# Optimization experiments

Measured on AMD Instinct MI355X. Metric: run time of the kernel, lower is better.

The kernel has to match this reference:

```python
import jax, jax.numpy as jnp
import numpy as np

BINS = 2048
DST_NBINS = 8
STEP = 1e-5


def _get_norm(delta_begin, delta_end, density):
    # integral of x^2 * density over [delta_begin, delta_end]
    return density * (delta_end ** 3 - delta_begin ** 3) / 3.0


def _quant_error(hist, bin_width, nsb, neb):
    # L2 quantization error of mapping src bins [nsb, neb] onto DST_NBINS bins
    dst_w = bin_width * (neb - nsb + 1).astype(jnp.float32) / DST_NBINS
    safe_w = jnp.where(dst_w == 0.0, 1.0, dst_w)
    src = jnp.arange(BINS, dtype=jnp.float32)
    begin = (src - nsb) * bin_width          # src bin left edge rel. to new range
    end = begin + bin_width
    db = jnp.clip(jnp.floor(begin / safe_w), 0, DST_NBINS - 1)
    de = jnp.clip(jnp.floor(end / safe_w), 0, DST_NBINS - 1)
    density = hist / bin_width
    db_c = (db + 0.5) * safe_w
    norm = _get_norm(begin - db_c, safe_w / 2, density)
    norm = norm + (de - db - 1.0) * _get_norm(-safe_w / 2, safe_w / 2, density)
    de_c = de * safe_w + safe_w / 2
    norm = norm + _get_norm(-safe_w / 2, end - de_c, density)
    return jnp.where(dst_w == 0.0, jnp.float32(0.0), norm.sum())


def _search(hist, min_val, max_val):
    # entropy-style greedy shrink of [start_bin, end_bin]; sequential, data-dependent
    bin_width = (max_val - min_val) / BINS
    total = hist.sum()
    cSum = jnp.cumsum(hist)

    def cond(s):
        alpha, beta, sb, eb, nm, done = s
        return (alpha < beta) & jnp.logical_not(done)

    def body(s):
        alpha, beta, sb, eb, nm, done = s
        na = alpha + STEP
        nb = beta - STEP
        # l: first bin (>= sb) with cSum >= na*total; r: last bin with cSum <= nb*total
        l = jnp.clip(jnp.searchsorted(cSum, na * total, side='left'), sb, eb)
        r = jnp.clip(jnp.searchsorted(cSum, nb * total, side='right') - 1, sb, eb)
        take_left = (l - sb) > (eb - r)
        nsb = jnp.where(take_left, l, sb)
        neb = jnp.where(take_left, eb, r)
        alpha2 = jnp.where(take_left, na, alpha)
        beta2 = jnp.where(take_left, beta, nb)
        changed = (nsb != sb) | (neb != eb)
        norm = _quant_error(hist, bin_width, nsb, neb)
        broke = changed & (norm > nm)
        accept = changed & jnp.logical_not(broke)
        return (alpha2, beta2,
                jnp.where(accept, nsb, sb),
                jnp.where(accept, neb, eb),
                jnp.where(accept, norm, nm),
                done | broke)

    init = (jnp.float32(0.0), jnp.float32(1.0),
            jnp.int32(0), jnp.int32(BINS - 1),
            jnp.float32(jnp.inf), jnp.bool_(False))
    _, _, sb, eb, _, _ = jax.lax.while_loop(cond, body, init)
    return sb, eb


def _forward(x):
    min_val = jnp.min(x)
    max_val = jnp.max(x)
    bin_width = (max_val - min_val) / BINS
    safe_bw = jnp.where(bin_width == 0.0, 1.0, bin_width)
    # torch.histc equivalent over [min_val, max_val]
    idx = jnp.clip(jnp.floor((x.ravel() - min_val) / safe_bw).astype(jnp.int32), 0, BINS - 1)
    hist = jnp.zeros(BINS, jnp.float32).at[idx].add(1.0)
    sb, eb = _search(jax.lax.stop_gradient(hist),
                     jax.lax.stop_gradient(min_val),
                     jax.lax.stop_gradient(max_val))
    new_min = min_val + bin_width * sb
    new_max = min_val + bin_width * (eb + 1)
    return jnp.stack([new_min, new_max])


def setup_inputs() -> dict:
    key = jax.random.key(0)
    x = jax.random.normal(key, (32, 1024, 1024), dtype=jnp.float32)
    return {"x": x}


def reference(x):
    return _forward(x)
```

## Files before the change

kernel.cpp:

```cpp
#include <hip/hip_runtime.h>
#include <float.h>
#include <math.h>

#define BINS 2048
#define DSTN 8
#define STEPF 1e-5f
#define NMM 1024
#define NHIST 512
#define MAXST 2048
#define NSEG 64
#define MINF 0x7fffffff
#define NT 1024

struct Ws {
  unsigned int mm_done, ev_done;
  int nseg, mbot;
  int n_states;
  int pad0[3];
  float min_val, max_val, bin_width, safe_bw;
  float pmin[NMM];
  float pmax[NMM];
  unsigned int hist[BINS];
  float histf[BINS];
  float Atab[2052];
  int   mterm[2052];
  int4  segB4[NSEG];
  float norms[MAXST];
  int2  states[MAXST];
};

__global__ void __launch_bounds__(256) k_minmax(const float* __restrict__ x, long long n,
                                                Ws* __restrict__ ws) {
  __shared__ float smin[4], smax[4];
  __shared__ float redn[256], redx[256];
  __shared__ __align__(16) int4 sB4[NSEG], sA4[NSEG];
  __shared__ int segklo[NSEG];
  __shared__ int s_nsg, s_mbot, s_nsa;
  __shared__ int amLast;
  int t = threadIdx.x;
  const float S = STEPF;

  if (blockIdx.x == NMM) {
    if (t == 0) {
      int sg = 0; float B = 1.0f; int m0 = 0; int mbot = MINF;
      while (sg < NSEG && B > 0.0f) {
        float Bn = B - S;
        if (Bn <= 0.0f) {
          sB4[sg] = make_int4(__float_as_int(B), __float_as_int(B - Bn), m0, 0);
          ++sg; mbot = m0 + 1; break;
        }
        float d = B - Bn;
        unsigned bb = __float_as_uint(B);
        unsigned bid = bb & 0x7f800000u;
        if ((bb & 0x007fffffu) == 0u) bid -= 0x00800000u;
        float binlo = __uint_as_float(bid);
        float brel = B - binlo;
        int nn = (int)floor((double)brel / (double)d);
        if (nn < 0) nn = 0;
        if (nn >= 2) {
          float B1 = B - d;
          float B2 = B1 - S;
          if (B1 - B2 != d) nn = 1;
        }
        sB4[sg] = make_int4(__float_as_int(B), __float_as_int(d), m0, nn);
        ++sg;
        float Blast = B - (float)nn * d;
        B = Blast - S;
        m0 += nn + 1;
        if (B <= 0.0f) { mbot = m0; break; }
      }
      s_nsg = sg; s_mbot = mbot;
      int sa = 0;
      sA4[sa++] = make_int4(__float_as_int(0.0f), __float_as_int(S), 0, 0);
      float A0 = S; int k0 = 1;
      while (sa < NSEG && k0 <= 2051) {
        float An = A0 + S;
        float d = An - A0;
        unsigned ab = __float_as_uint(A0);
        unsigned abid = ab & 0x7f800000u;
        float binhi = __uint_as_float(abid + 0x00800000u);
        float brel = binhi - A0;
        int nn = (int)floorf(brel / d);
        if (nn < 0) nn = 0;
        while (nn >= 1 && !(A0 + (float)nn * d < binhi)) --nn;
        while (A0 + (float)(nn + 1) * d < binhi) ++nn;
        if (nn >= 2) {
          float A1 = A0 + d;
          float A2 = A1 + S;
          if (A2 - A1 != d) nn = 1;
        }
        if (k0 + nn > 2051) nn = 2051 - k0;
        sA4[sa++] = make_int4(__float_as_int(A0), __float_as_int(d), k0, nn);
        float Alast = A0 + (float)nn * d;
        A0 = Alast + S;
        k0 += nn + 1;
      }
      s_nsa = sa;
    }
    __syncthreads();
    int nsg = s_nsg, mbot = s_mbot, nsa = s_nsa;

    for (int sg = 0; sg < nsa; ++sg) {
      int4 sv = sA4[sg];
      float A0v = __int_as_float(sv.x), dv = __int_as_float(sv.y);
      for (int i = t; i <= sv.w; i += 256) ws->Atab[sv.z + i] = A0v + (float)i * dv;
    }
    __syncthreads();
    {
      int okA = 1;
      for (int k = t; k < 2051; k += 256) okA &= (ws->Atab[k] + S == ws->Atab[k + 1]) ? 1 : 0;
      if (__syncthreads_and(okA) == 0) {
        if (t == 0) {
          float a = 0.0f; ws->Atab[0] = 0.0f;
          for (int k = 1; k < 2052; ++k) { a = a + S; ws->Atab[k] = a; }
        }
        __syncthreads();
      }
    }
    if (t < nsg) {
      int4 sv = sB4[t];
      float Bs = __int_as_float(sv.x), dd = __int_as_float(sv.y);
      float Bend = Bs - (float)sv.w * dd;
      int lo = 0, hi = 2052;
      while (lo < hi) { int mid = (lo + hi) >> 1; if (ws->Atab[mid] < Bend) lo = mid + 1; else hi = mid; }
      segklo[t] = lo;
      ws->segB4[t] = sv;
    }
    if (t == 0) { ws->nseg = nsg; ws->mbot = mbot; }
    __syncthreads();
    for (int sg = 0; sg < nsg; ++sg) {
      int lo = segklo[sg], hi = (sg ? segklo[sg - 1] : 2052);
      if (lo >= hi) continue;
      int4 sv = sB4[sg];
      float Bs = __int_as_float(sv.x), dd = __int_as_float(sv.y);
      int ms = sv.z, nn = sv.w;
      float rd = (dd > 0.0f) ? 1.0f / dd : 0.0f;
      for (int k = lo + t; k < hi; k += 256) {
        float a = ws->Atab[k];
        int i2 = (int)((Bs - a) * rd);
        if (i2 < 0) i2 = 0; if (i2 > nn) i2 = nn;
        while (i2 > 0 && Bs - (float)(i2 - 1) * dd <= a) --i2;
        while (i2 <= nn && Bs - (float)i2 * dd > a) ++i2;
        ws->mterm[k] = ms + i2;
      }
    }
    {
      int dhi = segklo[nsg - 1];
      for (int k = t; k < dhi; k += 256) ws->mterm[k] = mbot;
    }
    return;
  }

  long long n4 = n >> 2;
  float vmin = FLT_MAX, vmax = -FLT_MAX;
  const float4* __restrict__ x4 = (const float4*)x;
  long long stride = (long long)NMM * blockDim.x;
  for (long long i = (long long)blockIdx.x * blockDim.x + t; i < n4; i += stride) {
    float4 v = x4[i];
    vmin = fminf(vmin, fminf(fminf(v.x, v.y), fminf(v.z, v.w)));
    vmax = fmaxf(vmax, fmaxf(fmaxf(v.x, v.y), fmaxf(v.z, v.w)));
  }
  for (long long i = (n4 << 2) + (long long)blockIdx.x * blockDim.x + t; i < n; i += stride) {
    float v = x[i];
    vmin = fminf(vmin, v); vmax = fmaxf(vmax, v);
  }
  for (int off = 32; off > 0; off >>= 1) {
    vmin = fminf(vmin, __shfl_down(vmin, off));
    vmax = fmaxf(vmax, __shfl_down(vmax, off));
  }
  int wid = t >> 6;
  if ((t & 63) == 0) { smin[wid] = vmin; smax[wid] = vmax; }
  __syncthreads();
  if (t == 0) {
    float a = smin[0], b = smax[0];
    for (int w = 1; w < 4; ++w) { a = fminf(a, smin[w]); b = fmaxf(b, smax[w]); }
    ws->pmin[blockIdx.x] = a; ws->pmax[blockIdx.x] = b;
    __threadfence();
    amLast = (atomicAdd(&ws->mm_done, 1u) == (unsigned)(NMM - 1)) ? 1 : 0;
  }
  __syncthreads();
  if (amLast) {
    __threadfence();
    float fmn = FLT_MAX, fmx = -FLT_MAX;
    for (int i = t; i < NMM; i += 256) {
      fmn = fminf(fmn, ws->pmin[i]);
      fmx = fmaxf(fmx, ws->pmax[i]);
    }
    redn[t] = fmn; redx[t] = fmx;
    __syncthreads();
    for (int off = 128; off > 0; off >>= 1) {
      if (t < off) { redn[t] = fminf(redn[t], redn[t + off]); redx[t] = fmaxf(redx[t], redx[t + off]); }
      __syncthreads();
    }
    if (t == 0) {
      float mn = redn[0], mx = redx[0];
      ws->min_val = mn; ws->max_val = mx;
      float bw = (mx - mn) / (float)BINS;
      ws->bin_width = bw;
      ws->safe_bw = (bw == 0.0f) ? 1.0f : bw;
    }
    for (int i = t; i < BINS; i += 256) ws->hist[i] = 0u;
  }
}

__global__ void __launch_bounds__(256) k_hist(const float* __restrict__ x, long long n,
                                              Ws* __restrict__ ws) {
  __shared__ __align__(16) unsigned int lh[BINS * 4];
  for (int i = threadIdx.x; i < BINS * 4; i += 256) lh[i] = 0u;
  __syncthreads();
  float minv = ws->min_val;
  float sbw = ws->safe_bw;
  int sub = threadIdx.x & 3;
  long long n4 = n >> 2;
  const float4* __restrict__ x4 = (const float4*)x;
  long long stride = (long long)gridDim.x * blockDim.x;
  for (long long i = (long long)blockIdx.x * blockDim.x + threadIdx.x; i < n4; i += stride) {
    float4 v = x4[i];
    int a = (int)floorf((v.x - minv) / sbw);
    int b = (int)floorf((v.y - minv) / sbw);
    int c = (int)floorf((v.z - minv) / sbw);
    int d = (int)floorf((v.w - minv) / sbw);
    a = min(BINS - 1, max(0, a));
    b = min(BINS - 1, max(0, b));
    c = min(BINS - 1, max(0, c));
    d = min(BINS - 1, max(0, d));
    atomicAdd(&lh[(a << 2) | sub], 1u);
    atomicAdd(&lh[(b << 2) | sub], 1u);
    atomicAdd(&lh[(c << 2) | sub], 1u);
    atomicAdd(&lh[(d << 2) | sub], 1u);
  }
  for (long long i = (n4 << 2) + (long long)blockIdx.x * blockDim.x + threadIdx.x; i < n; i += stride) {
    int a = (int)floorf((x[i] - minv) / sbw);
    a = min(BINS - 1, max(0, a));
    atomicAdd(&lh[(a << 2) | sub], 1u);
  }
  __syncthreads();
  for (int i = threadIdx.x; i < BINS; i += 256) {
    uint4 v = *((const uint4*)lh + i);
    unsigned int c = v.x + v.y + v.z + v.w;
    if (c) atomicAdd(&ws->hist[i], c);
  }
}

__global__ void __launch_bounds__(NT) k_search(Ws* __restrict__ ws) {
  __shared__ __align__(16) float csum[BINS];
  __shared__ __align__(16) int2  ltmt[2052];
  __shared__ __align__(16) int   mcross[BINS];
  __shared__ __align__(16) int   chain[2052];
  __shared__ __align__(16) int2  ev[2049];
  __shared__ __align__(16) int4  sB4[NSEG];
  __shared__ int   segblo[NSEG];
  __shared__ float fwav[16];
  __shared__ int   ired[16], ired2[16];
  __shared__ int   pub_nc;
  __shared__ int   pub_mode, pub_j0, pub_sb, pub_mt, pub_nst0, pub_nfire, pub_clamp, pub_ntot;

  int t = threadIdx.x;
  int lane = t & 63, wid = t >> 6;

  if (t < NSEG) sB4[t] = ws->segB4[t];
  int nsg = ws->nseg;
  int mbot = ws->mbot;

  float h0 = (float)ws->hist[2 * t];
  float h1 = (float)ws->hist[2 * t + 1];
  ws->histf[2 * t] = h0; ws->histf[2 * t + 1] = h1;
  float s = h0 + h1;
  float isc = s;
  #pragma unroll
  for (int off = 1; off < 64; off <<= 1) {
    float u = __shfl_up(isc, off);
    if (lane >= off) isc += u;
  }
  if (lane == 63) fwav[wid] = isc;
  __syncthreads();
  if (t < 16) {
    float v = fwav[t];
    #pragma unroll
    for (int off = 1; off < 16; off <<= 1) {
      float u = __shfl_up(v, off, 16);
      if ((t & 15) >= off) v += u;
    }
    fwav[t] = v;
  }
  __syncthreads();
  {
    float base = wid ? fwav[wid - 1] : 0.0f;
    float excl = base + (isc - s);
    csum[2 * t] = excl + h0;
    csum[2 * t + 1] = excl + s;
  }
  __syncthreads();

  const float T = csum[BINS - 1];
  const float rcpT = 1.0f / T;

  {
    int lov[3], hiv[3];
    float av1[3];
    #pragma unroll
    for (int i = 0; i < 3; ++i) {
      int k = t + NT * i;
      bool has = (k <= 2050);
      lov[i] = 0; hiv[i] = has ? BINS : 0;
      av1[i] = has ? ws->Atab[k + 1] * T : 0.0f;
    }
    #pragma unroll
    for (int lev = 0; lev < 12; ++lev) {
      #pragma unroll
      for (int i = 0; i < 3; ++i) {
        bool act = lov[i] < hiv[i];
        int mid = act ? ((lov[i] + hiv[i]) >> 1) : 0;
        float cv = csum[mid];
        bool g = act && (cv < av1[i]);
        lov[i] = g ? (mid + 1) : lov[i];
        hiv[i] = (act && !g) ? mid : hiv[i];
      }
    }
    #pragma unroll
    for (int i = 0; i < 3; ++i) {
      int k = t + NT * i;
      if (k < 2052) ltmt[k] = make_int2((k <= 2050) ? lov[i] : BINS, ws->mterm[k]);
    }
  }
  if (t < nsg) {
    int4 sv = sB4[t];
    float Bs = __int_as_float(sv.x), dd = __int_as_float(sv.y);
    float Bend = Bs - (float)sv.w * dd;
    float vt = Bend * T;
    int lo = 0, hi = BINS;
    while (lo < hi) { int mid = (lo + hi) >> 1; if (!(csum[mid] > vt)) lo = mid + 1; else hi = mid; }
    segblo[t] = lo;
  }
  __syncthreads();

  for (int sg = 0; sg < nsg; ++sg) {
    int lo = segblo[sg], hi = (sg ? segblo[sg - 1] : BINS);
    if (lo >= hi) continue;
    int4 sv = sB4[sg];
    float Bs = __int_as_float(sv.x), dd = __int_as_float(sv.y);
    int ms = sv.z, nn = sv.w;
    float rd = (dd > 0.0f) ? 1.0f / dd : 0.0f;
    for (int b = lo + t; b < hi; b += NT) {
      float c = csum[b];
      int i2 = (int)((Bs - c * rcpT) * rd);
      if (i2 < 0) i2 = 0; if (i2 > nn) i2 = nn;
      while (i2 > 0 && (Bs - (float)(i2 - 1) * dd) * T < c) --i2;
      while (i2 <= nn && !((Bs - (float)i2 * dd) * T < c)) ++i2;
      mcross[b] = ms + i2 - 1;
    }
  }
  {
    int dhi = segblo[nsg - 1];
    for (int b = t; b < dhi; b += NT) {
      float c = csum[b];
      mcross[b] = (c > 0.0f) ? ((mbot == MINF) ? MINF : (mbot - 1)) : MINF;
    }
  }
  __syncthreads();

  {
    int b0 = 2 * t;
    int m0v = mcross[b0], m1v = mcross[b0 + 1];
    int mnext = (t < NT - 1) ? mcross[b0 + 2] : 0;
    bool e0b = (m0v != m1v);
    bool e1b = (b0 + 1 == BINS - 1) || (m1v != mnext);
    int cnt = (e0b ? 1 : 0) + (e1b ? 1 : 0);
    int inc = cnt;
    #pragma unroll
    for (int off = 1; off < 64; off <<= 1) {
      int u = __shfl_up(inc, off);
      if (lane >= off) inc += u;
    }
    if (lane == 63) ired[wid] = inc;
    __syncthreads();
    if (t < 16) {
      int v = ired[t];
      #pragma unroll
      for (int off = 1; off < 16; off <<= 1) {
        int u = __shfl_up(v, off, 16);
        if ((t & 15) >= off) v += u;
      }
      ired[t] = v;
    }
    __syncthreads();
    int base = wid ? ired[wid - 1] : 0;
    int incl_t = base + inc;
    int total = ired[15];
    int running = total - incl_t;
    if (e1b) { ++running; chain[running - 1] = b0 + 1; }
    if (e0b) { ++running; chain[running - 1] = b0; }
    if (t == 0) pub_nc = total;
  }
  __syncthreads();

  int NC = pub_nc;
  for (int j = 1 + t; j <= NC; j += NT) {
    ev[j] = make_int2(mcross[chain[j - 1]], (j < NC) ? chain[j] : -1);
  }
  if (t == 0 && NC < 2048) ev[NC + 1] = make_int2(MINF, -1);
  __syncthreads();

  if (t == 0) {
    int k = 0, sb = 0, eb = BINS - 1, m = 0, j = 1, nst = 0;
    int2 lm0 = ltmt[0], lm1 = ltmt[1], lm2 = ltmt[2];
    int2 e0 = ev[1], e1 = ev[2], e2 = ev[3];
    int mode = 0;
    int guard = 0;
    pub_j0 = 0; pub_sb = 0; pub_mt = 0;
    while (++guard < 6000) {
      int lpos = lm0.x, mt = lm0.y;
      int mc = e0.x, ne = e0.y;
      int l = min(lpos, eb);
      int pl = l - sb;
      if (pl <= 0) { mode = 1; pub_j0 = j; pub_sb = sb; pub_mt = mt; break; }
      if (m >= mt) break;
      bool coin = (m == mc);
      int nec = max(ne, sb);
      int pr = eb - nec;
      bool fl = !coin || (pl > pr);
      if (fl) {
        sb = l; ++k;
        if (nst < MAXST) ws->states[nst] = make_int2(sb, eb);
        ++nst;
        if (sb >= eb) break;
        lm0 = lm1; lm1 = lm2; lm2 = ltmt[min(k + 2, 2051)];
      } else {
        eb = nec; m = mc + 1; ++j;
        if (nst < MAXST) ws->states[nst] = make_int2(sb, eb);
        ++nst;
        if (sb >= eb) break;
        e0 = e1; e1 = e2; e2 = ev[min(j + 2, 2048)];
      }
    }
    pub_mode = mode;
    pub_nst0 = (nst < MAXST) ? nst : MAXST;
  }
  __syncthreads();

  int mode = pub_mode;
  int nst0 = pub_nst0;
  if (mode == 1) {
    int j0 = pub_j0, sbF = pub_sb, mtF = pub_mt;
    int locA = NC + 1, locB = NC + 1;
    for (int j = j0 + t; j <= NC; j += NT) {
      int2 e = ev[j];
      if (e.x >= mtF && j < locA) locA = j;
      if (e.y <= sbF && j < locB) locB = j;
    }
    #pragma unroll
    for (int off = 32; off > 0; off >>= 1) {
      locA = min(locA, __shfl_down(locA, off));
      locB = min(locB, __shfl_down(locB, off));
    }
    if (lane == 0) { ired[wid] = locA; ired2[wid] = locB; }
    __syncthreads();
    if (t == 0) {
      int jA = NC + 1, jB = NC + 1;
      for (int w = 0; w < 16; ++w) { jA = min(jA, ired[w]); jB = min(jB, ired2[w]); }
      int nfire, clampLast;
      if (jB < jA) { nfire = jB - j0 + 1; clampLast = 1; }
      else         { nfire = jA - j0;     clampLast = 0; }
      if (nfire < 0) nfire = 0;
      int ntot = nst0 + nfire;
      if (ntot > MAXST) ntot = MAXST;
      pub_nfire = nfire; pub_clamp = clampLast; pub_ntot = ntot;
    }
    __syncthreads();
    int nfire = pub_nfire, clampLast = pub_clamp;
    for (int i = t; i < nfire; i += NT) {
      int idx = nst0 + i;
      if (idx < MAXST) {
        int y = ev[j0 + i].y;
        ws->states[idx] = make_int2(sbF, (clampLast && i == nfire - 1) ? sbF : y);
      }
    }
    if (t == 0) ws->n_states = pub_ntot;
  } else {
    if (t == 0) ws->n_states = nst0;
  }
}

__global__ void __launch_bounds__(256) k_eval(Ws* __restrict__ ws) {
  int i = blockIdx.x;
  if (i >= ws->n_states) return;
  int2 st = ws->states[i];
  float bw = ws->bin_width;
  float cntf = (float)(st.y - st.x + 1);
  float w = bw * cntf / (float)DSTN;
  int t = threadIdx.x;
  if (w == 0.0f) {
    if (t == 0) ws->norms[i] = 0.0f;
    return;
  }
  float hw = 0.5f * w;
  float hw3 = hw * hw * hw;
  float nsb = (float)st.x;
  float sum = 0.0f;
  #pragma unroll
  for (int k = 0; k < 8; ++k) {
    int j = t + 256 * k;
    float h = ws->histf[j];
    float begin = ((float)j - nsb) * bw;
    float end = begin + bw;
    float db = fminf(fmaxf(floorf(begin / w), 0.0f), (float)(DSTN - 1));
    float de = fminf(fmaxf(floorf(end / w), 0.0f), (float)(DSTN - 1));
    float density = h / bw;
    float dbc = (db + 0.5f) * w;
    float a1 = begin - dbc;
    float n1 = density * (hw3 - a1 * a1 * a1) / 3.0f;
    float nmid = density * (hw3 + hw3) / 3.0f;
    float dec = de * w + hw;
    float a3 = end - dec;
    float n3 = density * (a3 * a3 * a3 + hw3) / 3.0f;
    sum += n1 + (de - db - 1.0f) * nmid + n3;
  }
  __shared__ float red[256];
  red[t] = sum;
  __syncthreads();
  for (int off = 128; off > 0; off >>= 1) {
    if (t < off) red[t] += red[t + off];
    __syncthreads();
  }
  if (t == 0) ws->norms[i] = red[0];
}

__global__ void __launch_bounds__(256) k_final(Ws* __restrict__ ws, float* __restrict__ out) {
  __shared__ int sbrk[256];
  int N = ws->n_states;
  int t = threadIdx.x;
  int loc = MINF;
  for (int i = t + 1; i < N; i += 256) {
    if (ws->norms[i] > ws->norms[i - 1]) loc = min(loc, i);
  }
  sbrk[t] = loc;
  __syncthreads();
  for (int off = 128; off > 0; off >>= 1) {
    if (t < off) sbrk[t] = min(sbrk[t], sbrk[t + off]);
    __syncthreads();
  }
  if (t == 0) {
    int sb, eb;
    if (N == 0) { sb = 0; eb = BINS - 1; }
    else {
      int ib = sbrk[0];
      int fi = (ib != MINF) ? (ib - 1) : (N - 1);
      int2 st = ws->states[fi];
      sb = st.x; eb = st.y;
    }
    float minv = ws->min_val, bw = ws->bin_width;
    out[0] = minv + bw * (float)sb;
    out[1] = minv + bw * (float)(eb + 1);
  }
}

extern "C" void kernel_launch(void* const* d_in, const int* in_sizes, int n_in,
                              void* d_out, int out_size, void* d_ws, size_t ws_size,
                              hipStream_t stream) {
  const float* x = (const float*)d_in[0];
  long long n = (long long)in_sizes[0];
  Ws* ws = (Ws*)d_ws;
  float* out = (float*)d_out;

  hipMemsetAsync(d_ws, 0, 8, stream);
  k_minmax<<<NMM + 1, 256, 0, stream>>>(x, n, ws);
  k_hist<<<NHIST, 256, 0, stream>>>(x, n, ws);
  k_search<<<1, NT, 0, stream>>>(ws);
  k_eval<<<MAXST, 256, 0, stream>>>(ws);
  k_final<<<1, 256, 0, stream>>>(ws, out);
}
```

Measured before the change: 165.2 us.

## Split table build into its own kernel and unroll min/max and histogram loads

The float-step table construction moves out of the extra k_minmax block into a separate single-block kernel launched first, so k_minmax no longer has one slow serial block holding up its tail. The min/max loop is unrolled four ways and the histogram loop two ways, so more independent float4 loads are in flight per thread. A reciprocal-multiply histogram variant is added but not launched. The launched k_hist_exact keeps the exact division. The cost is one more kernel launch, and the table kernel now runs serially ahead of the min/max pass.

```diff
diff --git a/kernel.cpp b/kernel.cpp
--- a/kernel.cpp
+++ b/kernel.cpp
@@ -29,139 +29,157 @@
   int2  states[MAXST];
 };
 
+__global__ void __launch_bounds__(256) k_tables(Ws* __restrict__ ws) {
+  __shared__ __align__(16) int4 sB4[NSEG], sA4[NSEG];
+  __shared__ int segklo[NSEG];
+  __shared__ int s_nsg, s_mbot, s_nsa;
+  int t = threadIdx.x;
+  const float S = STEPF;
+
+  if (t == 0) {
+    int sg = 0; float B = 1.0f; int m0 = 0; int mbot = MINF;
+    while (sg < NSEG && B > 0.0f) {
+      float Bn = B - S;
+      if (Bn <= 0.0f) {
+        sB4[sg] = make_int4(__float_as_int(B), __float_as_int(B - Bn), m0, 0);
+        ++sg; mbot = m0 + 1; break;
+      }
+      float d = B - Bn;
+      unsigned bb = __float_as_uint(B);
+      unsigned bid = bb & 0x7f800000u;
+      if ((bb & 0x007fffffu) == 0u) bid -= 0x00800000u;
+      float binlo = __uint_as_float(bid);
+      float brel = B - binlo;
+      int nn = (int)floor((double)brel / (double)d);
+      if (nn < 0) nn = 0;
+      if (nn >= 2) {
+        float B1 = B - d;
+        float B2 = B1 - S;
+        if (B1 - B2 != d) nn = 1;
+      }
+      sB4[sg] = make_int4(__float_as_int(B), __float_as_int(d), m0, nn);
+      ++sg;
+      float Blast = B - (float)nn * d;
+      B = Blast - S;
+      m0 += nn + 1;
+      if (B <= 0.0f) { mbot = m0; break; }
+    }
+    s_nsg = sg; s_mbot = mbot;
+    int sa = 0;
+    sA4[sa++] = make_int4(__float_as_int(0.0f), __float_as_int(S), 0, 0);
+    float A0 = S; int k0 = 1;
+    while (sa < NSEG && k0 <= 2051) {
+      float An = A0 + S;
+      float d = An - A0;
+      unsigned ab = __float_as_uint(A0);
+      unsigned abid = ab & 0x7f800000u;
+      float binhi = __uint_as_float(abid + 0x00800000u);
+      float brel = binhi - A0;
+      int nn = (int)floorf(brel / d);
+      if (nn < 0) nn = 0;
+      while (nn >= 1 && !(A0 + (float)nn * d < binhi)) --nn;
+      while (A0 + (float)(nn + 1) * d < binhi) ++nn;
+      if (nn >= 2) {
+        float A1 = A0 + d;
+        float A2 = A1 + S;
+        if (A2 - A1 != d) nn = 1;
+      }
+      if (k0 + nn > 2051) nn = 2051 - k0;
+      sA4[sa++] = make_int4(__float_as_int(A0), __float_as_int(d), k0, nn);
+      float Alast = A0 + (float)nn * d;
+      A0 = Alast + S;
+      k0 += nn + 1;
+    }
+    s_nsa = sa;
+  }
+  __syncthreads();
+  int nsg = s_nsg, mbot = s_mbot, nsa = s_nsa;
+
+  for (int sg = 0; sg < nsa; ++sg) {
+    int4 sv = sA4[sg];
+    float A0v = __int_as_float(sv.x), dv = __int_as_float(sv.y);
+    for (int i = t; i <= sv.w; i += 256) ws->Atab[sv.z + i] = A0v + (float)i * dv;
+  }
+  __syncthreads();
+  {
+    int okA = 1;
+    for (int k = t; k < 2051; k += 256) okA &= (ws->Atab[k] + S == ws->Atab[k + 1]) ? 1 : 0;
+    if (__syncthreads_and(okA) == 0) {
+      if (t == 0) {
+        float a = 0.0f; ws->Atab[0] = 0.0f;
+        for (int k = 1; k < 2052; ++k) { a = a + S; ws->Atab[k] = a; }
+      }
+      __syncthreads();
+    }
+  }
+  if (t < nsg) {
+    int4 sv = sB4[t];
+    float Bs = __int_as_float(sv.x), dd = __int_as_float(sv.y);
+    float Bend = Bs - (float)sv.w * dd;
+    int lo = 0, hi = 2052;
+    while (lo < hi) { int mid = (lo + hi) >> 1; if (ws->Atab[mid] < Bend) lo = mid + 1; else hi = mid; }
+    segklo[t] = lo;
+    ws->segB4[t] = sv;
+  }
+  if (t == 0) { ws->nseg = nsg; ws->mbot = mbot; }
+  __syncthreads();
+  for (int sg = 0; sg < nsg; ++sg) {
+    int lo = segklo[sg], hi = (sg ? segklo[sg - 1] : 2052);
+    if (lo >= hi) continue;
+    int4 sv = sB4[sg];
+    float Bs = __int_as_float(sv.x), dd = __int_as_float(sv.y);
+    int ms = sv.z, nn = sv.w;
+    float rd = (dd > 0.0f) ? 1.0f / dd : 0.0f;
+    for (int k = lo + t; k < hi; k += 256) {
+      float a = ws->Atab[k];
+      int i2 = (int)((Bs - a) * rd);
+      if (i2 < 0) i2 = 0; if (i2 > nn) i2 = nn;
+      while (i2 > 0 && Bs - (float)(i2 - 1) * dd <= a) --i2;
+      while (i2 <= nn && Bs - (float)i2 * dd > a) ++i2;
+      ws->mterm[k] = ms + i2;
+    }
+  }
+  {
+    int dhi = segklo[nsg - 1];
+    for (int k = t; k < dhi; k += 256) ws->mterm[k] = mbot;
+  }
+}
+
 __global__ void __launch_bounds__(256) k_minmax(const float* __restrict__ x, long long n,
                                                 Ws* __restrict__ ws) {
   __shared__ float smin[4], smax[4];
   __shared__ float redn[256], redx[256];
-  __shared__ __align__(16) int4 sB4[NSEG], sA4[NSEG];
-  __shared__ int segklo[NSEG];
-  __shared__ int s_nsg, s_mbot, s_nsa;
   __shared__ int amLast;
   int t = threadIdx.x;
-  const float S = STEPF;
-
-  if (blockIdx.x == NMM) {
-    if (t == 0) {
-      int sg = 0; float B = 1.0f; int m0 = 0; int mbot = MINF;
-      while (sg < NSEG && B > 0.0f) {
-        float Bn = B - S;
-        if (Bn <= 0.0f) {
-          sB4[sg] = make_int4(__float_as_int(B), __float_as_int(B - Bn), m0, 0);
-          ++sg; mbot = m0 + 1; break;
-        }
-        float d = B - Bn;
-        unsigned bb = __float_as_uint(B);
-        unsigned bid = bb & 0x7f800000u;
-        if ((bb & 0x007fffffu) == 0u) bid -= 0x00800000u;
-        float binlo = __uint_as_float(bid);
-        float brel = B - binlo;
-        int nn = (int)floor((double)brel / (double)d);
-        if (nn < 0) nn = 0;
-        if (nn >= 2) {
-          float B1 = B - d;
-          float B2 = B1 - S;
-          if (B1 - B2 != d) nn = 1;
-        }
-        sB4[sg] = make_int4(__float_as_int(B), __float_as_int(d), m0, nn);
-        ++sg;
-        float Blast = B - (float)nn * d;
-        B = Blast - S;
-        m0 += nn + 1;
-        if (B <= 0.0f) { mbot = m0; break; }
-      }
-      s_nsg = sg; s_mbot = mbot;
-      int sa = 0;
-      sA4[sa++] = make_int4(__float_as_int(0.0f), __float_as_int(S), 0, 0);
-      float A0 = S; int k0 = 1;
-      while (sa < NSEG && k0 <= 2051) {
-        float An = A0 + S;
-        float d = An - A0;
-        unsigned ab = __float_as_uint(A0);
-        unsigned abid = ab & 0x7f800000u;
-        float binhi = __uint_as_float(abid + 0x00800000u);
-        float brel = binhi - A0;
-        int nn = (int)floorf(brel / d);
-        if (nn < 0) nn = 0;
-        while (nn >= 1 && !(A0 + (float)nn * d < binhi)) --nn;
-        while (A0 + (float)(nn + 1) * d < binhi) ++nn;
-        if (nn >= 2) {
-          float A1 = A0 + d;
-          float A2 = A1 + S;
-          if (A2 - A1 != d) nn = 1;
-        }
-        if (k0 + nn > 2051) nn = 2051 - k0;
-        sA4[sa++] = make_int4(__float_as_int(A0), __float_as_int(d), k0, nn);
-        float Alast = A0 + (float)nn * d;
-        A0 = Alast + S;
-        k0 += nn + 1;
-      }
-      s_nsa = sa;
-    }
-    __syncthreads();
-    int nsg = s_nsg, mbot = s_mbot, nsa = s_nsa;
-
-    for (int sg = 0; sg < nsa; ++sg) {
-      int4 sv = sA4[sg];
-      float A0v = __int_as_float(sv.x), dv = __int_as_float(sv.y);
-      for (int i = t; i <= sv.w; i += 256) ws->Atab[sv.z + i] = A0v + (float)i * dv;
-    }
-    __syncthreads();
-    {
-      int okA = 1;
-      for (int k = t; k < 2051; k += 256) okA &= (ws->Atab[k] + S == ws->Atab[k + 1]) ? 1 : 0;
-      if (__syncthreads_and(okA) == 0) {
-        if (t == 0) {
-          float a = 0.0f; ws->Atab[0] = 0.0f;
-          for (int k = 1; k < 2052; ++k) { a = a + S; ws->Atab[k] = a; }
-        }
-        __syncthreads();
-      }
-    }
-    if (t < nsg) {
-      int4 sv = sB4[t];
-      float Bs = __int_as_float(sv.x), dd = __int_as_float(sv.y);
-      float Bend = Bs - (float)sv.w * dd;
-      int lo = 0, hi = 2052;
-      while (lo < hi) { int mid = (lo + hi) >> 1; if (ws->Atab[mid] < Bend) lo = mid + 1; else hi = mid; }
-      segklo[t] = lo;
-      ws->segB4[t] = sv;
-    }
-    if (t == 0) { ws->nseg = nsg; ws->mbot = mbot; }
-    __syncthreads();
-    for (int sg = 0; sg < nsg; ++sg) {
-      int lo = segklo[sg], hi = (sg ? segklo[sg - 1] : 2052);
-      if (lo >= hi) continue;
-      int4 sv = sB4[sg];
-      float Bs = __int_as_float(sv.x), dd = __int_as_float(sv.y);
-      int ms = sv.z, nn = sv.w;
-      float rd = (dd > 0.0f) ? 1.0f / dd : 0.0f;
-      for (int k = lo + t; k < hi; k += 256) {
-        float a = ws->Atab[k];
-        int i2 = (int)((Bs - a) * rd);
-        if (i2 < 0) i2 = 0; if (i2 > nn) i2 = nn;
-        while (i2 > 0 && Bs - (float)(i2 - 1) * dd <= a) --i2;
-        while (i2 <= nn && Bs - (float)i2 * dd > a) ++i2;
-        ws->mterm[k] = ms + i2;
-      }
-    }
-    {
-      int dhi = segklo[nsg - 1];
-      for (int k = t; k < dhi; k += 256) ws->mterm[k] = mbot;
-    }
-    return;
-  }
 
   long long n4 = n >> 2;
   float vmin = FLT_MAX, vmax = -FLT_MAX;
   const float4* __restrict__ x4 = (const float4*)x;
-  long long stride = (long long)NMM * blockDim.x;
-  for (long long i = (long long)blockIdx.x * blockDim.x + t; i < n4; i += stride) {
+  const long long stride = (long long)NMM * 256;
+  long long i = (long long)blockIdx.x * 256 + t;
+  for (; i + 3 * stride < n4; i += 4 * stride) {
+    float4 v0 = x4[i];
+    float4 v1 = x4[i + stride];
+    float4 v2 = x4[i + 2 * stride];
+    float4 v3 = x4[i + 3 * stride];
+    float mn0 = fminf(fminf(v0.x, v0.y), fminf(v0.z, v0.w));
+    float mx0 = fmaxf(fmaxf(v0.x, v0.y), fmaxf(v0.z, v0.w));
+    float mn1 = fminf(fminf(v1.x, v1.y), fminf(v1.z, v1.w));
+    float mx1 = fmaxf(fmaxf(v1.x, v1.y), fmaxf(v1.z, v1.w));
+    float mn2 = fminf(fminf(v2.x, v2.y), fminf(v2.z, v2.w));
+    float mx2 = fmaxf(fmaxf(v2.x, v2.y), fmaxf(v2.z, v2.w));
+    float mn3 = fminf(fminf(v3.x, v3.y), fminf(v3.z, v3.w));
+    float mx3 = fmaxf(fmaxf(v3.x, v3.y), fmaxf(v3.z, v3.w));
+    vmin = fminf(vmin, fminf(fminf(mn0, mn1), fminf(mn2, mn3)));
+    vmax = fmaxf(vmax, fmaxf(fmaxf(mx0, mx1), fmaxf(mx2, mx3)));
+  }
+  for (; i < n4; i += stride) {
     float4 v = x4[i];
     vmin = fminf(vmin, fminf(fminf(v.x, v.y), fminf(v.z, v.w)));
     vmax = fmaxf(vmax, fmaxf(fmaxf(v.x, v.y), fmaxf(v.z, v.w)));
   }
-  for (long long i = (n4 << 2) + (long long)blockIdx.x * blockDim.x + t; i < n; i += stride) {
-    float v = x[i];
+  for (long long q = (n4 << 2) + (long long)blockIdx.x * 256 + t; q < n; q += stride) {
+    float v = x[q];
     vmin = fminf(vmin, v); vmax = fmaxf(vmax, v);
   }
   for (int off = 32; off > 0; off >>= 1) {
@@ -182,9 +200,9 @@
   if (amLast) {
     __threadfence();
     float fmn = FLT_MAX, fmx = -FLT_MAX;
-    for (int i = t; i < NMM; i += 256) {
-      fmn = fminf(fmn, ws->pmin[i]);
-      fmx = fmaxf(fmx, ws->pmax[i]);
+    for (int q = t; q < NMM; q += 256) {
+      fmn = fminf(fmn, ws->pmin[q]);
+      fmx = fmaxf(fmx, ws->pmax[q]);
     }
     redn[t] = fmn; redx[t] = fmx;
     __syncthreads();
@@ -199,12 +217,70 @@
       ws->bin_width = bw;
       ws->safe_bw = (bw == 0.0f) ? 1.0f : bw;
     }
-    for (int i = t; i < BINS; i += 256) ws->hist[i] = 0u;
+    for (int q = t; q < BINS; q += 256) ws->hist[q] = 0u;
   }
 }
 
 __global__ void __launch_bounds__(256) k_hist(const float* __restrict__ x, long long n,
                                               Ws* __restrict__ ws) {
+  __shared__ __align__(16) unsigned int lh[BINS * 4];
+  for (int i = threadIdx.x; i < BINS * 4; i += 256) lh[i] = 0u;
+  __syncthreads();
+  float minv = ws->min_val;
+  float sbw = ws->safe_bw;
+  float rbw = 1.0f / sbw;
+  int sub = threadIdx.x & 3;
+  long long n4 = n >> 2;
+  const float4* __restrict__ x4 = (const float4*)x;
+  const long long stride = (long long)NHIST * 256;
+  long long i = (long long)blockIdx.x * 256 + threadIdx.x;
+  for (; i + stride < n4; i += 2 * stride) {
+    float4 v0 = x4[i];
+    float4 v1 = x4[i + stride];
+    int a0 = min(BINS - 1, max(0, (int)floorf((v0.x - minv) * rbw)));
+    int b0 = min(BINS - 1, max(0, (int)floorf((v0.y - minv) * rbw)));
+    int c0 = min(BINS - 1, max(0, (int)floorf((v0.z - minv) * rbw)));
+    int d0 = min(BINS - 1, max(0, (int)floorf((v0.w - minv) * rbw)));
+    int a1 = min(BINS - 1, max(0, (int)floorf((v1.x - minv) * rbw)));
+    int b1 = min(BINS - 1, max(0, (int)floorf((v1.y - minv) * rbw)));
+    int c1 = min(BINS - 1, max(0, (int)floorf((v1.z - minv) * rbw)));
+    int d1 = min(BINS - 1, max(0, (int)floorf((v1.w - minv) * rbw)));
+    atomicAdd(&lh[(a0 << 2) | sub], 1u);
+    atomicAdd(&lh[(b0 << 2) | sub], 1u);
+    atomicAdd(&lh[(c0 << 2) | sub], 1u);
+    atomicAdd(&lh[(d0 << 2) | sub], 1u);
+    atomicAdd(&lh[(a1 << 2) | sub], 1u);
+    atomicAdd(&lh[(b1 << 2) | sub], 1u);
+    atomicAdd(&lh[(c1 << 2) | sub], 1u);
+    atomicAdd(&lh[(d1 << 2) | sub], 1u);
+  }
+  for (; i < n4; i += stride) {
+    float4 v = x4[i];
+    int a = min(BINS - 1, max(0, (int)floorf((v.x - minv) * rbw)));
+    int b = min(BINS - 1, max(0, (int)floorf((v.y - minv) * rbw)));
+    int c = min(BINS - 1, max(0, (int)floorf((v.z - minv) * rbw)));
+    int d = min(BINS - 1, max(0, (int)floorf((v.w - minv) * rbw)));
+    atomicAdd(&lh[(a << 2) | sub], 1u);
+    atomicAdd(&lh[(b << 2) | sub], 1u);
+    atomicAdd(&lh[(c << 2) | sub], 1u);
+    atomicAdd(&lh[(d << 2) | sub], 1u);
+  }
+  for (long long q = (n4 << 2) + (long long)blockIdx.x * 256 + threadIdx.x; q < n; q += stride) {
+    int a = (int)floorf((x[q] - minv) / sbw);
+    a = min(BINS - 1, max(0, a));
+    atomicAdd(&lh[(a << 2) | sub], 1u);
+  }
+  __syncthreads();
+  for (int q = threadIdx.x; q < BINS; q += 256) {
+    uint4 v = *((const uint4*)lh + q);
+    unsigned int c = v.x + v.y + v.z + v.w;
+    if (c) atomicAdd(&ws->hist[q], c);
+  }
+}
+
+
+__global__ void __launch_bounds__(256) k_hist_exact(const float* __restrict__ x, long long n,
+                                                    Ws* __restrict__ ws) {
   __shared__ __align__(16) unsigned int lh[BINS * 4];
   for (int i = threadIdx.x; i < BINS * 4; i += 256) lh[i] = 0u;
   __syncthreads();
@@ -213,32 +289,49 @@
   int sub = threadIdx.x & 3;
   long long n4 = n >> 2;
   const float4* __restrict__ x4 = (const float4*)x;
-  long long stride = (long long)gridDim.x * blockDim.x;
-  for (long long i = (long long)blockIdx.x * blockDim.x + threadIdx.x; i < n4; i += stride) {
+  const long long stride = (long long)NHIST * 256;
+  long long i = (long long)blockIdx.x * 256 + threadIdx.x;
+  for (; i + stride < n4; i += 2 * stride) {
+    float4 v0 = x4[i];
+    float4 v1 = x4[i + stride];
+    int a0 = min(BINS - 1, max(0, (int)floorf((v0.x - minv) / sbw)));
+    int b0 = min(BINS - 1, max(0, (int)floorf((v0.y - minv) / sbw)));
+    int c0 = min(BINS - 1, max(0, (int)floorf((v0.z - minv) / sbw)));
+    int d0 = min(BINS - 1, max(0, (int)floorf((v0.w - minv) / sbw)));
+    int a1 = min(BINS - 1, max(0, (int)floorf((v1.x - minv) / sbw)));
+    int b1 = min(BINS - 1, max(0, (int)floorf((v1.y - minv) / sbw)));
+    int c1 = min(BINS - 1, max(0, (int)floorf((v1.z - minv) / sbw)));
+    int d1 = min(BINS - 1, max(0, (int)floorf((v1.w - minv) / sbw)));
+    atomicAdd(&lh[(a0 << 2) | sub], 1u);
+    atomicAdd(&lh[(b0 << 2) | sub], 1u);
+    atomicAdd(&lh[(c0 << 2) | sub], 1u);
+    atomicAdd(&lh[(d0 << 2) | sub], 1u);
+    atomicAdd(&lh[(a1 << 2) | sub], 1u);
+    atomicAdd(&lh[(b1 << 2) | sub], 1u);
+    atomicAdd(&lh[(c1 << 2) | sub], 1u);
+    atomicAdd(&lh[(d1 << 2) | sub], 1u);
+  }
+  for (; i < n4; i += stride) {
     float4 v = x4[i];
-    int a = (int)floorf((v.x - minv) / sbw);
-    int b = (int)floorf((v.y - minv) / sbw);
-    int c = (int)floorf((v.z - minv) / sbw);
-    int d = (int)floorf((v.w - minv) / sbw);
-    a = min(BINS - 1, max(0, a));
-    b = min(BINS - 1, max(0, b));
-    c = min(BINS - 1, max(0, c));
-    d = min(BINS - 1, max(0, d));
+    int a = min(BINS - 1, max(0, (int)floorf((v.x - minv) / sbw)));
+    int b = min(BINS - 1, max(0, (int)floorf((v.y - minv) / sbw)));
+    int c = min(BINS - 1, max(0, (int)floorf((v.z - minv) / sbw)));
+    int d = min(BINS - 1, max(0, (int)floorf((v.w - minv) / sbw)));
     atomicAdd(&lh[(a << 2) | sub], 1u);
     atomicAdd(&lh[(b << 2) | sub], 1u);
     atomicAdd(&lh[(c << 2) | sub], 1u);
     atomicAdd(&lh[(d << 2) | sub], 1u);
   }
-  for (long long i = (n4 << 2) + (long long)blockIdx.x * blockDim.x + threadIdx.x; i < n; i += stride) {
-    int a = (int)floorf((x[i] - minv) / sbw);
+  for (long long q = (n4 << 2) + (long long)blockIdx.x * 256 + threadIdx.x; q < n; q += stride) {
+    int a = (int)floorf((x[q] - minv) / sbw);
     a = min(BINS - 1, max(0, a));
     atomicAdd(&lh[(a << 2) | sub], 1u);
   }
   __syncthreads();
-  for (int i = threadIdx.x; i < BINS; i += 256) {
-    uint4 v = *((const uint4*)lh + i);
+  for (int q = threadIdx.x; q < BINS; q += 256) {
+    uint4 v = *((const uint4*)lh + q);
     unsigned int c = v.x + v.y + v.z + v.w;
-    if (c) atomicAdd(&ws->hist[i], c);
+    if (c) atomicAdd(&ws->hist[q], c);
   }
 }
 
@@ -563,8 +656,9 @@
   float* out = (float*)d_out;
 
   hipMemsetAsync(d_ws, 0, 8, stream);
-  k_minmax<<<NMM + 1, 256, 0, stream>>>(x, n, ws);
-  k_hist<<<NHIST, 256, 0, stream>>>(x, n, ws);
+  k_tables<<<1, 256, 0, stream>>>(ws);
+  k_minmax<<<NMM, 256, 0, stream>>>(x, n, ws);
+  k_hist_exact<<<NHIST, 256, 0, stream>>>(x, n, ws);
   k_search<<<1, NT, 0, stream>>>(ws);
   k_eval<<<MAXST, 256, 0, stream>>>(ws);
   k_final<<<1, 256, 0, stream>>>(ws, out);
```

Result: slower. 186.3 us (+12.8%).

## Split table build into own kernel; contiguous chunked, unrolled minmax and histogram loads

Applied to the files above, without the earlier changes.

Moves the serial table-construction work out of the minmax grid into its own single-block kernel, so the minmax blocks no longer wait on a straggler block. Both the minmax and histogram kernels now give each block one contiguous chunk and unroll the loads (8 and 4 float4 per iteration) to keep more memory requests in flight. NMM doubles to 2048 and launch bounds hint at 2 blocks per CU. The price is an extra kernel launch that runs serially before minmax, plus longer per-thread register live ranges.

```diff
diff --git a/kernel.cpp b/kernel.cpp
--- a/kernel.cpp
+++ b/kernel.cpp
@@ -5,7 +5,7 @@
 #define BINS 2048
 #define DSTN 8
 #define STEPF 1e-5f
-#define NMM 1024
+#define NMM 2048
 #define NHIST 512
 #define MAXST 2048
 #define NSEG 64
@@ -29,141 +29,180 @@
   int2  states[MAXST];
 };
 
-__global__ void __launch_bounds__(256) k_minmax(const float* __restrict__ x, long long n,
-                                                Ws* __restrict__ ws) {
-  __shared__ float smin[4], smax[4];
-  __shared__ float redn[256], redx[256];
+__global__ void __launch_bounds__(256) k_tables(Ws* __restrict__ ws) {
   __shared__ __align__(16) int4 sB4[NSEG], sA4[NSEG];
   __shared__ int segklo[NSEG];
   __shared__ int s_nsg, s_mbot, s_nsa;
+  int t = threadIdx.x;
+  const float S = STEPF;
+
+  if (t == 0) {
+    int sg = 0; float B = 1.0f; int m0 = 0; int mbot = MINF;
+    while (sg < NSEG && B > 0.0f) {
+      float Bn = B - S;
+      if (Bn <= 0.0f) {
+        sB4[sg] = make_int4(__float_as_int(B), __float_as_int(B - Bn), m0, 0);
+        ++sg; mbot = m0 + 1; break;
+      }
+      float d = B - Bn;
+      unsigned bb = __float_as_uint(B);
+      unsigned bid = bb & 0x7f800000u;
+      if ((bb & 0x007fffffu) == 0u) bid -= 0x00800000u;
+      float binlo = __uint_as_float(bid);
+      float brel = B - binlo;
+      int nn = (int)floor((double)brel / (double)d);
+      if (nn < 0) nn = 0;
+      if (nn >= 2) {
+        float B1 = B - d;
+        float B2 = B1 - S;
+        if (B1 - B2 != d) nn = 1;
+      }
+      sB4[sg] = make_int4(__float_as_int(B), __float_as_int(d), m0, nn);
+      ++sg;
+      float Blast = B - (float)nn * d;
+      B = Blast - S;
+      m0 += nn + 1;
+      if (B <= 0.0f) { mbot = m0; break; }
+    }
+    s_nsg = sg; s_mbot = mbot;
+    int sa = 0;
+    sA4[sa++] = make_int4(__float_as_int(0.0f), __float_as_int(S), 0, 0);
+    float A0 = S; int k0 = 1;
+    while (sa < NSEG && k0 <= 2051) {
+      float An = A0 + S;
+      float d = An - A0;
+      unsigned ab = __float_as_uint(A0);
+      unsigned abid = ab & 0x7f800000u;
+      float binhi = __uint_as_float(abid + 0x00800000u);
+      float brel = binhi - A0;
+      int nn = (int)floorf(brel / d);
+      if (nn < 0) nn = 0;
+      while (nn >= 1 && !(A0 + (float)nn * d < binhi)) --nn;
+      while (A0 + (float)(nn + 1) * d < binhi) ++nn;
+      if (nn >= 2) {
+        float A1 = A0 + d;
+        float A2 = A1 + S;
+        if (A2 - A1 != d) nn = 1;
+      }
+      if (k0 + nn > 2051) nn = 2051 - k0;
+      sA4[sa++] = make_int4(__float_as_int(A0), __float_as_int(d), k0, nn);
+      float Alast = A0 + (float)nn * d;
+      A0 = Alast + S;
+      k0 += nn + 1;
+    }
+    s_nsa = sa;
+  }
+  __syncthreads();
+  int nsg = s_nsg, mbot = s_mbot, nsa = s_nsa;
+
+  for (int sg = 0; sg < nsa; ++sg) {
+    int4 sv = sA4[sg];
+    float A0v = __int_as_float(sv.x), dv = __int_as_float(sv.y);
+    for (int i = t; i <= sv.w; i += 256) ws->Atab[sv.z + i] = A0v + (float)i * dv;
+  }
+  __syncthreads();
+  {
+    int okA = 1;
+    for (int k = t; k < 2051; k += 256) okA &= (ws->Atab[k] + S == ws->Atab[k + 1]) ? 1 : 0;
+    if (__syncthreads_and(okA) == 0) {
+      if (t == 0) {
+        float a = 0.0f; ws->Atab[0] = 0.0f;
+        for (int k = 1; k < 2052; ++k) { a = a + S; ws->Atab[k] = a; }
+      }
+      __syncthreads();
+    }
+  }
+  if (t < nsg) {
+    int4 sv = sB4[t];
+    float Bs = __int_as_float(sv.x), dd = __int_as_float(sv.y);
+    float Bend = Bs - (float)sv.w * dd;
+    int lo = 0, hi = 2052;
+    while (lo < hi) { int mid = (lo + hi) >> 1; if (ws->Atab[mid] < Bend) lo = mid + 1; else hi = mid; }
+    segklo[t] = lo;
+    ws->segB4[t] = sv;
+  }
+  if (t == 0) { ws->nseg = nsg; ws->mbot = mbot; }
+  __syncthreads();
+  for (int sg = 0; sg < nsg; ++sg) {
+    int lo = segklo[sg], hi = (sg ? segklo[sg - 1] : 2052);
+    if (lo >= hi) continue;
+    int4 sv = sB4[sg];
+    float Bs = __int_as_float(sv.x), dd = __int_as_float(sv.y);
+    int ms = sv.z, nn = sv.w;
+    float rd = (dd > 0.0f) ? 1.0f / dd : 0.0f;
+    for (int k = lo + t; k < hi; k += 256) {
+      float a = ws->Atab[k];
+      int i2 = (int)((Bs - a) * rd);
+      if (i2 < 0) i2 = 0; if (i2 > nn) i2 = nn;
+      while (i2 > 0 && Bs - (float)(i2 - 1) * dd <= a) --i2;
+      while (i2 <= nn && Bs - (float)i2 * dd > a) ++i2;
+      ws->mterm[k] = ms + i2;
+    }
+  }
+  {
+    int dhi = segklo[nsg - 1];
+    for (int k = t; k < dhi; k += 256) ws->mterm[k] = mbot;
+  }
+}
+
+__global__ void __launch_bounds__(256, 2) k_minmax(const float* __restrict__ x, long long n,
+                                                   Ws* __restrict__ ws) {
+  __shared__ float smin[4], smax[4];
+  __shared__ float redn[256], redx[256];
   __shared__ int amLast;
   int t = threadIdx.x;
-  const float S = STEPF;
-
-  if (blockIdx.x == NMM) {
-    if (t == 0) {
-      int sg = 0; float B = 1.0f; int m0 = 0; int mbot = MINF;
-      while (sg < NSEG && B > 0.0f) {
-        float Bn = B - S;
-        if (Bn <= 0.0f) {
-          sB4[sg] = make_int4(__float_as_int(B), __float_as_int(B - Bn), m0, 0);
-          ++sg; mbot = m0 + 1; break;
-        }
-        float d = B - Bn;
-        unsigned bb = __float_as_uint(B);
-        unsigned bid = bb & 0x7f800000u;
-        if ((bb & 0x007fffffu) == 0u) bid -= 0x00800000u;
-        float binlo = __uint_as_float(bid);
-        float brel = B - binlo;
-        int nn = (int)floor((double)brel / (double)d);
-        if (nn < 0) nn = 0;
-        if (nn >= 2) {
-          float B1 = B - d;
-          float B2 = B1 - S;
-          if (B1 - B2 != d) nn = 1;
-        }
-        sB4[sg] = make_int4(__float_as_int(B), __float_as_int(d), m0, nn);
-        ++sg;
-        float Blast = B - (float)nn * d;
-        B = Blast - S;
-        m0 += nn + 1;
-        if (B <= 0.0f) { mbot = m0; break; }
-      }
-      s_nsg = sg; s_mbot = mbot;
-      int sa = 0;
-      sA4[sa++] = make_int4(__float_as_int(0.0f), __float_as_int(S), 0, 0);
-      float A0 = S; int k0 = 1;
-      while (sa < NSEG && k0 <= 2051) {
-        float An = A0 + S;
-        float d = An - A0;
-        unsigned ab = __float_as_uint(A0);
-        unsigned abid = ab & 0x7f800000u;
-        float binhi = __uint_as_float(abid + 0x00800000u);
-        float brel = binhi - A0;
-        int nn = (int)floorf(brel / d);
-        if (nn < 0) nn = 0;
-        while (nn >= 1 && !(A0 + (float)nn * d < binhi)) --nn;
-        while (A0 + (float)(nn + 1) * d < binhi) ++nn;
-        if (nn >= 2) {
-          float A1 = A0 + d;
-          float A2 = A1 + S;
-          if (A2 - A1 != d) nn = 1;
-        }
-        if (k0 + nn > 2051) nn = 2051 - k0;
-        sA4[sa++] = make_int4(__float_as_int(A0), __float_as_int(d), k0, nn);
-        float Alast = A0 + (float)nn * d;
-        A0 = Alast + S;
-        k0 += nn + 1;
-      }
-      s_nsa = sa;
-    }
-    __syncthreads();
-    int nsg = s_nsg, mbot = s_mbot, nsa = s_nsa;
-
-    for (int sg = 0; sg < nsa; ++sg) {
-      int4 sv = sA4[sg];
-      float A0v = __int_as_float(sv.x), dv = __int_as_float(sv.y);
-      for (int i = t; i <= sv.w; i += 256) ws->Atab[sv.z + i] = A0v + (float)i * dv;
-    }
-    __syncthreads();
-    {
-      int okA = 1;
-      for (int k = t; k < 2051; k += 256) okA &= (ws->Atab[k] + S == ws->Atab[k + 1]) ? 1 : 0;
-      if (__syncthreads_and(okA) == 0) {
-        if (t == 0) {
-          float a = 0.0f; ws->Atab[0] = 0.0f;
-          for (int k = 1; k < 2052; ++k) { a = a + S; ws->Atab[k] = a; }
-        }
-        __syncthreads();
-      }
-    }
-    if (t < nsg) {
-      int4 sv = sB4[t];
-      float Bs = __int_as_float(sv.x), dd = __int_as_float(sv.y);
-      float Bend = Bs - (float)sv.w * dd;
-      int lo = 0, hi = 2052;
-      while (lo < hi) { int mid = (lo + hi) >> 1; if (ws->Atab[mid] < Bend) lo = mid + 1; else hi = mid; }
-      segklo[t] = lo;
-      ws->segB4[t] = sv;
-    }
-    if (t == 0) { ws->nseg = nsg; ws->mbot = mbot; }
-    __syncthreads();
-    for (int sg = 0; sg < nsg; ++sg) {
-      int lo = segklo[sg], hi = (sg ? segklo[sg - 1] : 2052);
-      if (lo >= hi) continue;
-      int4 sv = sB4[sg];
-      float Bs = __int_as_float(sv.x), dd = __int_as_float(sv.y);
-      int ms = sv.z, nn = sv.w;
-      float rd = (dd > 0.0f) ? 1.0f / dd : 0.0f;
-      for (int k = lo + t; k < hi; k += 256) {
-        float a = ws->Atab[k];
-        int i2 = (int)((Bs - a) * rd);
-        if (i2 < 0) i2 = 0; if (i2 > nn) i2 = nn;
-        while (i2 > 0 && Bs - (float)(i2 - 1) * dd <= a) --i2;
-        while (i2 <= nn && Bs - (float)i2 * dd > a) ++i2;
-        ws->mterm[k] = ms + i2;
-      }
-    }
-    {
-      int dhi = segklo[nsg - 1];
-      for (int k = t; k < dhi; k += 256) ws->mterm[k] = mbot;
-    }
-    return;
-  }
 
   long long n4 = n >> 2;
+  const float4* __restrict__ x4 = (const float4*)x;
+  long long chunk = (n4 + NMM - 1) / NMM;
+  long long end = (long long)(blockIdx.x + 1) * chunk;
+  if (end > n4) end = n4;
+  long long i = (long long)blockIdx.x * chunk + t;
   float vmin = FLT_MAX, vmax = -FLT_MAX;
-  const float4* __restrict__ x4 = (const float4*)x;
-  long long stride = (long long)NMM * blockDim.x;
-  for (long long i = (long long)blockIdx.x * blockDim.x + t; i < n4; i += stride) {
+
+  for (; i + 7 * 256 < end; i += 8 * 256) {
+    float4 v0 = x4[i];
+    float4 v1 = x4[i + 256];
+    float4 v2 = x4[i + 512];
+    float4 v3 = x4[i + 768];
+    float4 v4 = x4[i + 1024];
+    float4 v5 = x4[i + 1280];
+    float4 v6 = x4[i + 1536];
+    float4 v7 = x4[i + 1792];
+    float mn0 = fminf(fminf(v0.x, v0.y), fminf(v0.z, v0.w));
+    float mn1 = fminf(fminf(v1.x, v1.y), fminf(v1.z, v1.w));
+    float mn2 = fminf(fminf(v2.x, v2.y), fminf(v2.z, v2.w));
+    float mn3 = fminf(fminf(v3.x, v3.y), fminf(v3.z, v3.w));
+    float mn4 = fminf(fminf(v4.x, v4.y), fminf(v4.z, v4.w));
+    float mn5 = fminf(fminf(v5.x, v5.y), fminf(v5.z, v5.w));
+    float mn6 = fminf(fminf(v6.x, v6.y), fminf(v6.z, v6.w));
+    float mn7 = fminf(fminf(v7.x, v7.y), fminf(v7.z, v7.w));
+    float mx0 = fmaxf(fmaxf(v0.x, v0.y), fmaxf(v0.z, v0.w));
+    float mx1 = fmaxf(fmaxf(v1.x, v1.y), fmaxf(v1.z, v1.w));
+    float mx2 = fmaxf(fmaxf(v2.x, v2.y), fmaxf(v2.z, v2.w));
+    float mx3 = fmaxf(fmaxf(v3.x, v3.y), fmaxf(v3.z, v3.w));
+    float mx4 = fmaxf(fmaxf(v4.x, v4.y), fmaxf(v4.z, v4.w));
+    float mx5 = fmaxf(fmaxf(v5.x, v5.y), fmaxf(v5.z, v5.w));
+    float mx6 = fmaxf(fmaxf(v6.x, v6.y), fmaxf(v6.z, v6.w));
+    float mx7 = fmaxf(fmaxf(v7.x, v7.y), fmaxf(v7.z, v7.w));
+    vmin = fminf(vmin, fminf(fminf(fminf(mn0, mn1), fminf(mn2, mn3)),
+                             fminf(fminf(mn4, mn5), fminf(mn6, mn7))));
+    vmax = fmaxf(vmax, fmaxf(fmaxf(fmaxf(mx0, mx1), fmaxf(mx2, mx3)),
+                             fmaxf(fmaxf(mx4, mx5), fmaxf(mx6, mx7))));
+  }
+  for (; i < end; i += 256) {
     float4 v = x4[i];
     vmin = fminf(vmin, fminf(fminf(v.x, v.y), fminf(v.z, v.w)));
     vmax = fmaxf(vmax, fmaxf(fmaxf(v.x, v.y), fmaxf(v.z, v.w)));
   }
-  for (long long i = (n4 << 2) + (long long)blockIdx.x * blockDim.x + t; i < n; i += stride) {
-    float v = x[i];
-    vmin = fminf(vmin, v); vmax = fmaxf(vmax, v);
-  }
+  if (blockIdx.x == 0) {
+    int rem = (int)(n - (n4 << 2));
+    if (t < rem) {
+      float v = x[(n4 << 2) + t];
+      vmin = fminf(vmin, v); vmax = fmaxf(vmax, v);
+    }
+  }
+
   for (int off = 32; off > 0; off >>= 1) {
     vmin = fminf(vmin, __shfl_down(vmin, off));
     vmax = fmaxf(vmax, __shfl_down(vmax, off));
@@ -182,9 +221,9 @@
   if (amLast) {
     __threadfence();
     float fmn = FLT_MAX, fmx = -FLT_MAX;
-    for (int i = t; i < NMM; i += 256) {
-      fmn = fminf(fmn, ws->pmin[i]);
-      fmx = fmaxf(fmx, ws->pmax[i]);
+    for (int q = t; q < NMM; q += 256) {
+      fmn = fminf(fmn, ws->pmin[q]);
+      fmx = fmaxf(fmx, ws->pmax[q]);
     }
     redn[t] = fmn; redx[t] = fmx;
     __syncthreads();
@@ -199,46 +238,88 @@
       ws->bin_width = bw;
       ws->safe_bw = (bw == 0.0f) ? 1.0f : bw;
     }
-    for (int i = t; i < BINS; i += 256) ws->hist[i] = 0u;
+    for (int q = t; q < BINS; q += 256) ws->hist[q] = 0u;
   }
 }
 
-__global__ void __launch_bounds__(256) k_hist(const float* __restrict__ x, long long n,
-                                              Ws* __restrict__ ws) {
+__global__ void __launch_bounds__(256, 2) k_hist(const float* __restrict__ x, long long n,
+                                                 Ws* __restrict__ ws) {
   __shared__ __align__(16) unsigned int lh[BINS * 4];
   for (int i = threadIdx.x; i < BINS * 4; i += 256) lh[i] = 0u;
   __syncthreads();
   float minv = ws->min_val;
   float sbw = ws->safe_bw;
   int sub = threadIdx.x & 3;
+  int t = threadIdx.x;
   long long n4 = n >> 2;
   const float4* __restrict__ x4 = (const float4*)x;
-  long long stride = (long long)gridDim.x * blockDim.x;
-  for (long long i = (long long)blockIdx.x * blockDim.x + threadIdx.x; i < n4; i += stride) {
+  long long chunk = (n4 + NHIST - 1) / NHIST;
+  long long end = (long long)(blockIdx.x + 1) * chunk;
+  if (end > n4) end = n4;
+  long long i = (long long)blockIdx.x * chunk + t;
+
+  for (; i + 3 * 256 < end; i += 4 * 256) {
+    float4 v0 = x4[i];
+    float4 v1 = x4[i + 256];
+    float4 v2 = x4[i + 512];
+    float4 v3 = x4[i + 768];
+    int a0 = min(BINS - 1, max(0, (int)floorf((v0.x - minv) / sbw)));
+    int b0 = min(BINS - 1, max(0, (int)floorf((v0.y - minv) / sbw)));
+    int c0 = min(BINS - 1, max(0, (int)floorf((v0.z - minv) / sbw)));
+    int d0 = min(BINS - 1, max(0, (int)floorf((v0.w - minv) / sbw)));
+    int a1 = min(BINS - 1, max(0, (int)floorf((v1.x - minv) / sbw)));
+    int b1 = min(BINS - 1, max(0, (int)floorf((v1.y - minv) / sbw)));
+    int c1 = min(BINS - 1, max(0, (int)floorf((v1.z - minv) / sbw)));
+    int d1 = min(BINS - 1, max(0, (int)floorf((v1.w - minv) / sbw)));
+    int a2 = min(BINS - 1, max(0, (int)floorf((v2.x - minv) / sbw)));
+    int b2 = min(BINS - 1, max(0, (int)floorf((v2.y - minv) / sbw)));
+    int c2 = min(BINS - 1, max(0, (int)floorf((v2.z - minv) / sbw)));
+    int d2 = min(BINS - 1, max(0, (int)floorf((v2.w - minv) / sbw)));
+    int a3 = min(BINS - 1, max(0, (int)floorf((v3.x - minv) / sbw)));
+    int b3 = min(BINS - 1, max(0, (int)floorf((v3.y - minv) / sbw)));
+    int c3 = min(BINS - 1, max(0, (int)floorf((v3.z - minv) / sbw)));
+    int d3 = min(BINS - 1, max(0, (int)floorf((v3.w - minv) / sbw)));
+    atomicAdd(&lh[(a0 << 2) | sub], 1u);
+    atomicAdd(&lh[(b0 << 2) | sub], 1u);
+    atomicAdd(&lh[(c0 << 2) | sub], 1u);
+    atomicAdd(&lh[(d0 << 2) | sub], 1u);
+    atomicAdd(&lh[(a1 << 2) | sub], 1u);
+    atomicAdd(&lh[(b1 << 2) | sub], 1u);
+    atomicAdd(&lh[(c1 << 2) | sub], 1u);
+    atomicAdd(&lh[(d1 << 2) | sub], 1u);
+    atomicAdd(&lh[(a2 << 2) | sub], 1u);
+    atomicAdd(&lh[(b2 << 2) | sub], 1u);
+    atomicAdd(&lh[(c2 << 2) | sub], 1u);
+    atomicAdd(&lh[(d2 << 2) | sub], 1u);
+    atomicAdd(&lh[(a3 << 2) | sub], 1u);
+    atomicAdd(&lh[(b3 << 2) | sub], 1u);
+    atomicAdd(&lh[(c3 << 2) | sub], 1u);
+    atomicAdd(&lh[(d3 << 2) | sub], 1u);
+  }
+  for (; i < end; i += 256) {
     float4 v = x4[i];
-    int a = (int)floorf((v.x - minv) / sbw);
-    int b = (int)floorf((v.y - minv) / sbw);
-    int c = (int)floorf((v.z - minv) / sbw);
-    int d = (int)floorf((v.w - minv) / sbw);
-    a = min(BINS - 1, max(0, a));
-    b = min(BINS - 1, max(0, b));
-    c = min(BINS - 1, max(0, c));
-    d = min(BINS - 1, max(0, d));
+    int a = min(BINS - 1, max(0, (int)floorf((v.x - minv) / sbw)));
+    int b = min(BINS - 1, max(0, (int)floorf((v.y - minv) / sbw)));
+    int c = min(BINS - 1, max(0, (int)floorf((v.z - minv) / sbw)));
+    int d = min(BINS - 1, max(0, (int)floorf((v.w - minv) / sbw)));
     atomicAdd(&lh[(a << 2) | sub], 1u);
     atomicAdd(&lh[(b << 2) | sub], 1u);
     atomicAdd(&lh[(c << 2) | sub], 1u);
     atomicAdd(&lh[(d << 2) | sub], 1u);
   }
-  for (long long i = (n4 << 2) + (long long)blockIdx.x * blockDim.x + threadIdx.x; i < n; i += stride) {
-    int a = (int)floorf((x[i] - minv) / sbw);
-    a = min(BINS - 1, max(0, a));
-    atomicAdd(&lh[(a << 2) | sub], 1u);
-  }
-  __syncthreads();
-  for (int i = threadIdx.x; i < BINS; i += 256) {
-    uint4 v = *((const uint4*)lh + i);
+  if (blockIdx.x == 0) {
+    int rem = (int)(n - (n4 << 2));
+    if (t < rem) {
+      int a = (int)floorf((x[(n4 << 2) + t] - minv) / sbw);
+      a = min(BINS - 1, max(0, a));
+      atomicAdd(&lh[(a << 2) | sub], 1u);
+    }
+  }
+  __syncthreads();
+  for (int q = threadIdx.x; q < BINS; q += 256) {
+    uint4 v = *((const uint4*)lh + q);
     unsigned int c = v.x + v.y + v.z + v.w;
-    if (c) atomicAdd(&ws->hist[i], c);
+    if (c) atomicAdd(&ws->hist[q], c);
   }
 }
 
@@ -563,7 +644,8 @@
   float* out = (float*)d_out;
 
   hipMemsetAsync(d_ws, 0, 8, stream);
-  k_minmax<<<NMM + 1, 256, 0, stream>>>(x, n, ws);
+  k_tables<<<1, 256, 0, stream>>>(ws);
+  k_minmax<<<NMM, 256, 0, stream>>>(x, n, ws);
   k_hist<<<NHIST, 256, 0, stream>>>(x, n, ws);
   k_search<<<1, NT, 0, stream>>>(ws);
   k_eval<<<MAXST, 256, 0, stream>>>(ws);
```

Measured after the change: 220.1 us. 1.33x slower.
